# Kernel optimization log

Hardware: AMD Instinct MI355X
Metric: run time of the kernel (lower is better)

Reference implementation:

```python
import jax, jax.numpy as jnp
import numpy as np

ALPHA = 0.2  # LeakyReLU negative slope
NEG_INF = -9e15


def _gat_layer(Wh, adj, a, concat):
    """One GraphAttentionLayer given pre-projected Wh [B,N,F].
    Algebraic split of the concat attention: e[b,i,j] = lrelu(Wh[i]@a1 + Wh[j]@a2),
    identical math to matmul(cat(Wh_i, Wh_j), a)."""
    F_ = Wh.shape[-1]
    f1 = Wh @ a[:F_, 0]   # [B,N]
    f2 = Wh @ a[F_:, 0]   # [B,N]
    e = jax.nn.leaky_relu(f1[:, :, None] + f2[:, None, :], negative_slope=ALPHA)  # [B,N,N]
    e = jnp.where(adj > 0, e, NEG_INF)
    att = jax.nn.softmax(e, axis=-1)            # dropout omitted (eval mode)
    h_prime = jnp.einsum('bij,bjf->bif', att, Wh)
    return jax.nn.elu(h_prime) if concat else h_prime


def setup_inputs() -> dict:
    key = jax.random.key(0)
    ks = jax.random.split(key, 9)
    B, N, Fin, H, nH, Fout = 4, 2048, 512, 128, 4, 256
    x = jax.random.normal(ks[0], (B, N, Fin), dtype=jnp.float32)
    adj = jax.random.randint(ks[1], (B, N, N), 0, 2, dtype=jnp.int32)
    mask = jnp.ones((B, N), dtype=jnp.float32)
    s = 0.05
    W_heads = jax.random.normal(ks[2], (nH, Fin, H), dtype=jnp.float32) * s
    a_heads = jax.random.normal(ks[3], (nH, 2 * H, 1), dtype=jnp.float32) * s
    W_out = jax.random.normal(ks[4], (nH * H, Fout), dtype=jnp.float32) * s
    a_out = jax.random.normal(ks[5], (2 * Fout, 1), dtype=jnp.float32) * s
    W_pool = jax.random.normal(ks[6], (Fout, Fout), dtype=jnp.float32) * s
    b_pool = jax.random.normal(ks[7], (Fout,), dtype=jnp.float32) * s
    return {"x": x, "adj": adj, "mask": mask, "W_heads": W_heads, "a_heads": a_heads,
            "W_out": W_out, "a_out": a_out, "W_pool": W_pool, "b_pool": b_pool}


def reference(x, adj, mask, W_heads, a_heads, W_out, a_out, W_pool, b_pool):
    # multi-head GAT layer, heads concatenated (dropout = identity in eval)
    heads = [_gat_layer(x @ W_heads[h], adj, a_heads[h], concat=True)
             for h in range(W_heads.shape[0])]
    xcat = jnp.concatenate(heads, axis=-1)                 # [B,N,nH*H]
    x_out = _gat_layer(xcat @ W_out, adj, a_out, concat=False)  # [B,N,Fout]
    x_out = x_out * mask[:, :, None]
    pooled = x_out.sum(axis=1) / (mask.sum(axis=1, keepdims=True) + 1e-10)
    graph_embedding = jax.nn.relu(pooled @ W_pool + b_pool)
    return graph_embedding, x_out
```

## Files before the change

kernel.cpp:

```cpp
#include <hip/hip_runtime.h>

typedef unsigned short u16;
typedef __attribute__((ext_vector_type(8))) short s8v;
typedef __attribute__((ext_vector_type(8))) unsigned short us8;
typedef __attribute__((ext_vector_type(4))) float f4v;

#define L2E 1.4426950408889634f

typedef __attribute__((address_space(1))) void gvoid_t;
typedef __attribute__((address_space(3))) void lvoid_t;

__device__ __forceinline__ u16 f2bf(float f) {
  unsigned u = __builtin_bit_cast(unsigned, f);
  return (u16)((u + 0x7FFFu + ((u >> 16) & 1u)) >> 16);
}
__device__ __forceinline__ float bf2f(u16 h) {
  return __builtin_bit_cast(float, ((unsigned)h) << 16);
}
__device__ __forceinline__ f4v mfma16(s8v a, s8v b, f4v c) {
  return __builtin_amdgcn_mfma_f32_16x16x32_bf16(a, b, c, 0, 0, 0);
}
__device__ __forceinline__ float exp2fast(float x) {
#if __has_builtin(__builtin_amdgcn_exp2f)
  return __builtin_amdgcn_exp2f(x);
#else
  return exp2f(x);
#endif
}
__device__ __forceinline__ void stage16(const u16* g, u16* lds_arr, int slot) {
#if __has_builtin(__builtin_amdgcn_global_load_lds)
  __builtin_amdgcn_global_load_lds((gvoid_t*)(g),
      (lvoid_t*)(lds_arr + (size_t)(slot & ~63) * 8), 16, 0, 0);
#else
  *(us8*)(lds_arr + (size_t)slot * 8) = *(const us8*)g;
#endif
}

__global__ __launch_bounds__(256) void prep_x(const float* __restrict__ x,
                                              u16* __restrict__ xb) {
  int i = (blockIdx.x * 256 + threadIdx.x) * 8;
  float4 v0 = *(const float4*)(x + i);
  float4 v1 = *(const float4*)(x + i + 4);
  us8 o;
  o[0] = f2bf(v0.x); o[1] = f2bf(v0.y); o[2] = f2bf(v0.z); o[3] = f2bf(v0.w);
  o[4] = f2bf(v1.x); o[5] = f2bf(v1.y); o[6] = f2bf(v1.z); o[7] = f2bf(v1.w);
  *(us8*)(xb + i) = o;
}

__global__ __launch_bounds__(256) void prep_wall(const float* __restrict__ W,
                                                 u16* __restrict__ Wt) {
  int idx = blockIdx.x * 256 + threadIdx.x;
  int h = idx >> 16, k = (idx >> 7) & 511, f = idx & 127;
  Wt[(size_t)(h * 128 + f) * 512 + k] = f2bf(W[idx]);
}
__global__ __launch_bounds__(256) void prep_wout(const float* __restrict__ W,
                                                 u16* __restrict__ Wt) {
  int idx = blockIdx.x * 256 + threadIdx.x;
  int k = idx >> 8, c = idx & 255;
  Wt[(size_t)c * 512 + k] = f2bf(W[idx]);
}
__global__ __launch_bounds__(256) void prep_adj(const int* __restrict__ adj,
                                                unsigned* __restrict__ adjw) {
  int chunk = blockIdx.x * 4 + (threadIdx.x >> 6);
  int l = threadIdx.x & 63;
  int v = adj[(size_t)chunk * 64 + l];
  unsigned long long m = __ballot(v != 0);
  if (l == 0) {
    ((uint2*)adjw)[chunk] = make_uint2((unsigned)m, (unsigned)(m >> 32));
  }
}

__global__ __launch_bounds__(256) void gemm_bf16(const u16* __restrict__ A,
                                                 const u16* __restrict__ Bt,
                                                 u16* __restrict__ Ct, int CO) {
  const int K = 512, N = 2048;
  int m0 = blockIdx.x * 128;
  int n0 = blockIdx.y * 128;
  int t = threadIdx.x;
  int w = t >> 6, l = t & 63, lr = l & 15, lq = l >> 4;
  int wr = w >> 1, wc = w & 1;
  __shared__ u16 As[2][128 * 32];
  __shared__ u16 Bs[2][128 * 32];
  f4v zero4 = {0.f, 0.f, 0.f, 0.f};
  f4v acc[4][4];
#pragma unroll
  for (int i = 0; i < 4; ++i)
#pragma unroll
    for (int j = 0; j < 4; ++j) acc[i][j] = zero4;

  auto stage = [&](int buf, int kt) {
    int k0 = kt * 32;
    int row = t >> 2, ch = t & 3;
    stage16(A + (size_t)(m0 + row) * K + k0 + ch * 8, As[buf], t);
    stage16(Bt + (size_t)(n0 + row) * K + k0 + ch * 8, Bs[buf], t);
    int s2 = t + 256;
    row = s2 >> 2; ch = s2 & 3;
    stage16(A + (size_t)(m0 + row) * K + k0 + ch * 8, As[buf], s2);
    stage16(Bt + (size_t)(n0 + row) * K + k0 + ch * 8, Bs[buf], s2);
  };
  stage(0, 0);
  for (int kt = 0; kt < 16; ++kt) {
    __syncthreads();
    if (kt < 15) stage((kt + 1) & 1, kt + 1);
    const u16* as = As[kt & 1];
    const u16* bs = Bs[kt & 1];
    s8v af[4], bfr[4];
#pragma unroll
    for (int rf = 0; rf < 4; ++rf)
      af[rf] = *(const s8v*)&as[(wr * 64 + rf * 16 + lr) * 32 + lq * 8];
#pragma unroll
    for (int nf = 0; nf < 4; ++nf)
      bfr[nf] = *(const s8v*)&bs[(wc * 64 + nf * 16 + lr) * 32 + lq * 8];
#pragma unroll
    for (int rf = 0; rf < 4; ++rf)
#pragma unroll
      for (int nf = 0; nf < 4; ++nf)
        acc[rf][nf] = mfma16(af[rf], bfr[nf], acc[rf][nf]);
  }
  int bidx = m0 >> 11;
  int nr0 = m0 & 2047;
#pragma unroll
  for (int rf = 0; rf < 4; ++rf) {
#pragma unroll
    for (int nf = 0; nf < 4; ++nf) {
      int col = n0 + wc * 64 + nf * 16 + lr;
      int nr = nr0 + wr * 64 + rf * 16 + lq * 4;
      f4v a = acc[rf][nf];
      ushort4 v = make_ushort4(f2bf(a[0]), f2bf(a[1]), f2bf(a[2]), f2bf(a[3]));
      *(ushort4*)&Ct[((size_t)bidx * CO + col) * N + nr] = v;
    }
  }
}

__global__ __launch_bounds__(256) void fkern(const u16* __restrict__ Wht,
                                             const float* __restrict__ a,
                                             float* __restrict__ f1L,
                                             float* __restrict__ f2L, int COLS,
                                             int F) {
  const int N = 2048;
  int h = blockIdx.z, b = blockIdx.y;
  int nl = threadIdx.x & 63, fc = threadIdx.x >> 6;
  int n = blockIdx.x * 64 + nl;
  int F4 = F >> 2;
  const u16* colp = Wht + ((size_t)(b * COLS + h * F + fc * F4)) * N + n;
  const float* ah = a + h * 2 * F + fc * F4;
  float a1 = 0.f, a2 = 0.f;
  for (int c = 0; c < F4; ++c) {
    float v = bf2f(colp[(size_t)c * N]);
    a1 = fmaf(v, ah[c], a1);
    a2 = fmaf(v, ah[F + c], a2);
  }
  __shared__ float r1[4][64], r2[4][64];
  r1[fc][nl] = a1;
  r2[fc][nl] = a2;
  __syncthreads();
  if (fc == 0) {
    float s1 = r1[0][nl] + r1[1][nl] + r1[2][nl] + r1[3][nl];
    float s2 = r2[0][nl] + r2[1][nl] + r2[2][nl] + r2[3][nl];
    f1L[(size_t)(h * 4 + b) * N + n] = s1 * L2E;
    f2L[(size_t)(h * 4 + b) * N + n] = s2 * L2E;
  }
}

__global__ __launch_bounds__(256) void fmax_kern(const float* __restrict__ f2L,
                                                 float* __restrict__ f2m) {
  int row = blockIdx.x;
  const float* p = f2L + (size_t)row * 2048;
  int t = threadIdx.x;
  float v = -__builtin_inff();
  for (int k = 0; k < 8; ++k) v = fmaxf(v, p[t + k * 256]);
#pragma unroll
  for (int d = 1; d < 64; d <<= 1) v = fmaxf(v, __shfl_xor(v, d));
  __shared__ float wm[4];
  if ((t & 63) == 0) wm[t >> 6] = v;
  __syncthreads();
  if (t == 0) f2m[row] = fmaxf(fmaxf(wm[0], wm[1]), fmaxf(wm[2], wm[3]));
}

template <int CT, bool ELU>
__global__ __launch_bounds__(256, 2) void attn_kernel(
    const u16* __restrict__ Wht, const float* __restrict__ f1L,
    const float* __restrict__ f2L, const float* __restrict__ f2max,
    const unsigned* __restrict__ adjw, const float* __restrict__ mask,
    void* __restrict__ outp) {
  const int N = 2048;
  constexpr int NCH = CT / 128;
  constexpr int ROWS = 64;
  constexpr int NT = 2048 / ROWS;
  constexpr int FHD = (CT == 512) ? 1 : 0;
  int kb = blockIdx.x;
  int x = kb & 7, g = kb >> 3;
  int p = x + 8 * (g / NT);
  int it = g % NT;
  int b = p / NCH, ch = p % NCH;
  int i0 = it * ROWS, col0 = ch * 128;
  int fh = FHD ? ch : 0;
  int t = threadIdx.x;
  int w = t >> 6, l = t & 63, lr = l & 15, lq = l >> 4;

  __shared__ u16 Vs[2][128 * 64];
  __shared__ unsigned adjs[ROWS * 65];
  __shared__ float f2s[2048];

  const float* f1p = f1L + (size_t)(fh * 4 + b) * N + i0;
  const float* f2p = f2L + (size_t)(fh * 4 + b) * N;
  float f2m = f2max[fh * 4 + b];
  float f1v = f1p[w * 16 + lr];
  float su = f1v + f2m;
  float M = fmaxf(su, 0.2f * su);
  float c1 = f1v - M;
  float c2 = 0.2f * f1v - M;
  const u16* vbase = Wht + (size_t)(b * CT + col0) * 2048;

  for (int i = t; i < ROWS * 64; i += 256) {
    int row = i >> 6, wd = i & 63;
    adjs[row * 65 + wd] = adjw[(size_t)(b * N + i0 + row) * 64 + wd];
  }
  for (int i = t; i < 2048; i += 256) f2s[i] = f2p[i];

  auto stage = [&](int buf, int kt) {
    int k0 = kt * 64;
#pragma unroll
    for (int j2 = 0; j2 < 4; ++j2) {
      int s = j2 * 256 + t;
      int c = s >> 3, q = s & 7;
      stage16(vbase + (size_t)c * 2048 + k0 + q * 8, Vs[buf], s);
    }
  };
  stage(0, 0);

  f4v zero4 = {0.f, 0.f, 0.f, 0.f};
  f4v acc[8];
#pragma unroll
  for (int j = 0; j < 8; ++j) acc[j] = zero4;
  float s_ = 0.f;

  for (int kt = 0; kt < 32; ++kt) {
    __syncthreads();
    if (kt < 31) stage((kt + 1) & 1, kt + 1);
    const u16* vs = Vs[kt & 1];
#pragma unroll
    for (int kk = 0; kk < 2; ++kk) {
      int jt = kt * 2 + kk;
      s8v vf[8];
#pragma unroll
      for (int nf = 0; nf < 8; ++nf)
        vf[nf] = *(const s8v*)&vs[(nf * 16 + lr) * 64 + kk * 32 + lq * 8];
      float4 fa = *(const float4*)&f2s[jt * 32 + lq * 8];
      float4 fb = *(const float4*)&f2s[jt * 32 + lq * 8 + 4];
      float f2c[8] = {fa.x, fa.y, fa.z, fa.w, fb.x, fb.y, fb.z, fb.w};
      unsigned aw = adjs[(w * 16 + lr) * 65 + jt];
      union { s8v v; unsigned u[4]; } pk;
#pragma unroll
      for (int ep = 0; ep < 4; ++ep) {
        float t1 = c1 + f2c[2 * ep];
        float t2 = fmaf(0.2f, f2c[2 * ep], c2);
        float p0 = exp2fast(fmaxf(t1, t2));
        p0 = ((aw >> (lq * 8 + 2 * ep)) & 1u) ? p0 : 0.f;
        s_ += p0;
        float t3 = c1 + f2c[2 * ep + 1];
        float t4 = fmaf(0.2f, f2c[2 * ep + 1], c2);
        float p1 = exp2fast(fmaxf(t3, t4));
        p1 = ((aw >> (lq * 8 + 2 * ep + 1)) & 1u) ? p1 : 0.f;
        s_ += p1;
        asm("v_cvt_pk_bf16_f32 %0, %1, %2"
            : "=v"(pk.u[ep]) : "v"(p0), "v"(p1));
      }
      s8v pa = pk.v;
#pragma unroll
      for (int nf = 0; nf < 8; ++nf)
        acc[nf] = mfma16(pa, vf[nf], acc[nf]);
    }
  }
  s_ += __shfl_xor(s_, 16);
  s_ += __shfl_xor(s_, 32);
  float inv = 1.f / fmaxf(s_, 1e-30f);
  f4v i4;
#pragma unroll
  for (int r = 0; r < 4; ++r) i4[r] = __shfl(inv, lq * 4 + r);
  int rowb = i0 + w * 16 + lq * 4;
#pragma unroll
  for (int nf = 0; nf < 8; ++nf) {
    int col = col0 + nf * 16 + lr;
#pragma unroll
    for (int r = 0; r < 4; ++r) {
      float v = acc[nf][r] * i4[r];
      size_t ob = (size_t)(b * N + rowb + r) * CT + col;
      if constexpr (ELU) {
        v = v > 0.f ? v : exp2fast(v * L2E) - 1.f;
        ((u16*)outp)[ob] = f2bf(v);
      } else {
        ((float*)outp)[ob] = v * mask[b * N + rowb + r];
      }
    }
  }
}

__global__ __launch_bounds__(256) void pool1(const float* __restrict__ xout,
                                             const float* __restrict__ mask,
                                             float* __restrict__ pool,
                                             float* __restrict__ den) {
  int b = blockIdx.x >> 6, s = blockIdx.x & 63;
  int c = threadIdx.x;
  int n0 = s * 32;
  float acc = 0.f;
  for (int r = 0; r < 32; ++r)
    acc += xout[((size_t)(b * 2048 + n0 + r)) * 256 + c];
  atomicAdd(&pool[b * 256 + c], acc);
  if (c == 0) {
    float ms = 0.f;
    for (int r = 0; r < 32; ++r) ms += mask[b * 2048 + n0 + r];
    atomicAdd(&den[b], ms);
  }
}
__global__ __launch_bounds__(256) void pool2(const float* __restrict__ pool,
                                             const float* __restrict__ den,
                                             const float* __restrict__ Wp,
                                             const float* __restrict__ bp,
                                             float* __restrict__ out) {
  int b = blockIdx.x, f = threadIdx.x;
  __shared__ float pv[256];
  float inv = 1.f / (den[b] + 1e-10f);
  pv[f] = pool[b * 256 + f] * inv;
  __syncthreads();
  float acc = bp[f];
  for (int c = 0; c < 256; ++c) acc = fmaf(pv[c], Wp[c * 256 + f], acc);
  out[b * 256 + f] = fmaxf(acc, 0.f);
}

extern "C" void kernel_launch(void* const* d_in, const int* in_sizes, int n_in,
                              void* d_out, int out_size, void* d_ws,
                              size_t ws_size, hipStream_t stream) {
  (void)in_sizes; (void)n_in; (void)out_size; (void)ws_size;
  const float* x = (const float*)d_in[0];
  const int* adj = (const int*)d_in[1];
  const float* mask = (const float*)d_in[2];
  const float* Whds = (const float*)d_in[3];
  const float* ahds = (const float*)d_in[4];
  const float* Wout = (const float*)d_in[5];
  const float* aout = (const float*)d_in[6];
  const float* Wpool = (const float*)d_in[7];
  const float* bpool = (const float*)d_in[8];
  float* out = (float*)d_out;

  char* ws = (char*)d_ws;
  size_t off = 0;
  auto take = [&](size_t n) {
    char* p = ws + off;
    off += (n + 255) & ~(size_t)255;
    return p;
  };
  u16* xb = (u16*)take(8192ull * 512 * 2);
  u16* Wta = (u16*)take(512ull * 512 * 2);
  u16* Wto = (u16*)take(256ull * 512 * 2);
  unsigned* adjw = (unsigned*)take(4ull * 2048 * 64 * 4);
  u16* Wht = (u16*)take(4ull * 512 * 2048 * 2);
  float* f1a = (float*)take(4ull * 4 * 2048 * 4);
  float* f2a = (float*)take(4ull * 4 * 2048 * 4);
  u16* xcat = (u16*)take(8192ull * 512 * 2);
  u16* Wh2t = (u16*)take(4ull * 256 * 2048 * 2);
  float* f1b = (float*)take(4ull * 2048 * 4);
  float* f2b = (float*)take(4ull * 2048 * 4);
  float* f2ma = (float*)take(16 * 4);
  float* f2mb = (float*)take(4 * 4);
  float* pool = (float*)take(1024 * 4);
  float* den = (float*)take(256);

  prep_x<<<2048, 256, 0, stream>>>(x, xb);
  prep_wall<<<1024, 256, 0, stream>>>(Whds, Wta);
  prep_wout<<<512, 256, 0, stream>>>(Wout, Wto);
  prep_adj<<<65536, 256, 0, stream>>>(adj, adjw);
  gemm_bf16<<<dim3(64, 4), 256, 0, stream>>>(xb, Wta, Wht, 512);
  fkern<<<dim3(32, 4, 4), 256, 0, stream>>>(Wht, ahds, f1a, f2a, 512, 128);
  fmax_kern<<<16, 256, 0, stream>>>(f2a, f2ma);
  attn_kernel<512, true><<<512, 256, 0, stream>>>(Wht, f1a, f2a, f2ma,
                                                  adjw, nullptr, xcat);
  gemm_bf16<<<dim3(64, 2), 256, 0, stream>>>(xcat, Wto, Wh2t, 256);
  fkern<<<dim3(32, 4, 1), 256, 0, stream>>>(Wh2t, aout, f1b, f2b, 256, 256);
  fmax_kern<<<4, 256, 0, stream>>>(f2b, f2mb);
  attn_kernel<256, false><<<256, 256, 0, stream>>>(Wh2t, f1b, f2b, f2mb,
                                                   adjw, mask, out + 1024);
  hipMemsetAsync(pool, 0, 4096 + 256, stream);
  pool1<<<256, 256, 0, stream>>>(out + 1024, mask, pool, den);
  pool2<<<4, 256, 0, stream>>>(pool, den, Wpool, bpool, out);
}
```

Baseline: 196.4 us.

## Split attention over the neighbour dimension across wave groups and swizzle LDS tiles

The attention kernel now runs 512-thread blocks in which groups of waves each handle a slice of the neighbour (j) range for the same rows. Partial accumulators and row sums are combined through LDS atomics before normalisation and a vectorised store. The second-layer attention now launches 512 blocks with fewer rows each, to raise parallelism. Both the GEMM and the attention V tiles use an XOR swizzle on the 16-byte chunk index to avoid LDS bank conflicts, and f2 is read straight from global memory instead of being staged in LDS. The costs are the extra reduction step, the LDS atomics and more LDS per block.

```diff
diff --git a/kernel.cpp b/kernel.cpp
--- a/kernel.cpp
+++ b/kernel.cpp
@@ -91,14 +91,17 @@
   auto stage = [&](int buf, int kt) {
     int k0 = kt * 32;
     int row = t >> 2, ch = t & 3;
-    stage16(A + (size_t)(m0 + row) * K + k0 + ch * 8, As[buf], t);
-    stage16(Bt + (size_t)(n0 + row) * K + k0 + ch * 8, Bs[buf], t);
+    int q = (ch ^ ((row >> 1) & 3)) * 8;
+    stage16(A + (size_t)(m0 + row) * K + k0 + q, As[buf], t);
+    stage16(Bt + (size_t)(n0 + row) * K + k0 + q, Bs[buf], t);
     int s2 = t + 256;
     row = s2 >> 2; ch = s2 & 3;
-    stage16(A + (size_t)(m0 + row) * K + k0 + ch * 8, As[buf], s2);
-    stage16(Bt + (size_t)(n0 + row) * K + k0 + ch * 8, Bs[buf], s2);
+    q = (ch ^ ((row >> 1) & 3)) * 8;
+    stage16(A + (size_t)(m0 + row) * K + k0 + q, As[buf], s2);
+    stage16(Bt + (size_t)(n0 + row) * K + k0 + q, Bs[buf], s2);
   };
   stage(0, 0);
+  int swz = (lq ^ ((lr >> 1) & 3)) * 8;
   for (int kt = 0; kt < 16; ++kt) {
     __syncthreads();
     if (kt < 15) stage((kt + 1) & 1, kt + 1);
@@ -107,10 +110,10 @@
     s8v af[4], bfr[4];
 #pragma unroll
     for (int rf = 0; rf < 4; ++rf)
-      af[rf] = *(const s8v*)&as[(wr * 64 + rf * 16 + lr) * 32 + lq * 8];
+      af[rf] = *(const s8v*)&as[(wr * 64 + rf * 16 + lr) * 32 + swz];
 #pragma unroll
     for (int nf = 0; nf < 4; ++nf)
-      bfr[nf] = *(const s8v*)&bs[(wc * 64 + nf * 16 + lr) * 32 + lq * 8];
+      bfr[nf] = *(const s8v*)&bs[(wc * 64 + nf * 16 + lr) * 32 + swz];
 #pragma unroll
     for (int rf = 0; rf < 4; ++rf)
 #pragma unroll
@@ -177,16 +180,19 @@
   if (t == 0) f2m[row] = fmaxf(fmaxf(wm[0], wm[1]), fmaxf(wm[2], wm[3]));
 }
 
-template <int CT, bool ELU>
-__global__ __launch_bounds__(256, 2) void attn_kernel(
+template <int CT, int WPJ, bool ELU>
+__global__ __launch_bounds__(512, 4) void attn_kernel(
     const u16* __restrict__ Wht, const float* __restrict__ f1L,
     const float* __restrict__ f2L, const float* __restrict__ f2max,
     const unsigned* __restrict__ adjw, const float* __restrict__ mask,
     void* __restrict__ outp) {
   const int N = 2048;
   constexpr int NCH = CT / 128;
-  constexpr int ROWS = 64;
+  constexpr int ROWS = WPJ * 16;
   constexpr int NT = 2048 / ROWS;
+  constexpr int NJ = 8 / WPJ;
+  constexpr int JR = 2048 / NJ;
+  constexpr int KT = JR / 32;
   constexpr int FHD = (CT == 512) ? 1 : 0;
   int kb = blockIdx.x;
   int x = kb & 7, g = kb >> 3;
@@ -197,34 +203,40 @@
   int fh = FHD ? ch : 0;
   int t = threadIdx.x;
   int w = t >> 6, l = t & 63, lr = l & 15, lq = l >> 4;
-
-  __shared__ u16 Vs[2][128 * 64];
+  int jg = w / WPJ, ws = w % WPJ;
+  int tg = t & (WPJ * 64 - 1);
+
+  __shared__ __attribute__((aligned(16))) u16 Vs[NJ * 2 * 4096];
   __shared__ unsigned adjs[ROWS * 65];
-  __shared__ float f2s[2048];
+  __shared__ float sum_lds[ROWS];
+  float* accm = (float*)Vs;
 
   const float* f1p = f1L + (size_t)(fh * 4 + b) * N + i0;
   const float* f2p = f2L + (size_t)(fh * 4 + b) * N;
   float f2m = f2max[fh * 4 + b];
-  float f1v = f1p[w * 16 + lr];
+  float f1v = f1p[ws * 16 + lr];
   float su = f1v + f2m;
   float M = fmaxf(su, 0.2f * su);
   float c1 = f1v - M;
   float c2 = 0.2f * f1v - M;
   const u16* vbase = Wht + (size_t)(b * CT + col0) * 2048;
-
-  for (int i = t; i < ROWS * 64; i += 256) {
+  int j0g = jg * JR;
+
+  for (int i = t; i < ROWS * 64; i += 512) {
     int row = i >> 6, wd = i & 63;
     adjs[row * 65 + wd] = adjw[(size_t)(b * N + i0 + row) * 64 + wd];
   }
-  for (int i = t; i < 2048; i += 256) f2s[i] = f2p[i];
-
+  u16* vg0 = &Vs[(jg * 2 + 0) * 4096];
+  u16* vg1 = &Vs[(jg * 2 + 1) * 4096];
   auto stage = [&](int buf, int kt) {
-    int k0 = kt * 64;
-#pragma unroll
-    for (int j2 = 0; j2 < 4; ++j2) {
-      int s = j2 * 256 + t;
-      int c = s >> 3, q = s & 7;
-      stage16(vbase + (size_t)c * 2048 + k0 + q * 8, Vs[buf], s);
+    u16* dst = buf ? vg1 : vg0;
+    int k0 = j0g + kt * 32;
+#pragma unroll
+    for (int j2 = 0; j2 < 512 / (WPJ * 64); ++j2) {
+      int s = j2 * (WPJ * 64) + tg;
+      int c = s >> 2, q = s & 3;
+      stage16(vbase + (size_t)c * 2048 + k0 + (q ^ ((c >> 1) & 3)) * 8, dst,
+              s);
     }
   };
   stage(0, 0);
@@ -234,64 +246,82 @@
 #pragma unroll
   for (int j = 0; j < 8; ++j) acc[j] = zero4;
   float s_ = 0.f;
-
-  for (int kt = 0; kt < 32; ++kt) {
+  int chn = lq ^ ((lr >> 1) & 3);
+
+  for (int kt = 0; kt < KT; ++kt) {
     __syncthreads();
-    if (kt < 31) stage((kt + 1) & 1, kt + 1);
-    const u16* vs = Vs[kt & 1];
-#pragma unroll
-    for (int kk = 0; kk < 2; ++kk) {
-      int jt = kt * 2 + kk;
-      s8v vf[8];
-#pragma unroll
-      for (int nf = 0; nf < 8; ++nf)
-        vf[nf] = *(const s8v*)&vs[(nf * 16 + lr) * 64 + kk * 32 + lq * 8];
-      float4 fa = *(const float4*)&f2s[jt * 32 + lq * 8];
-      float4 fb = *(const float4*)&f2s[jt * 32 + lq * 8 + 4];
-      float f2c[8] = {fa.x, fa.y, fa.z, fa.w, fb.x, fb.y, fb.z, fb.w};
-      unsigned aw = adjs[(w * 16 + lr) * 65 + jt];
-      union { s8v v; unsigned u[4]; } pk;
-#pragma unroll
-      for (int ep = 0; ep < 4; ++ep) {
-        float t1 = c1 + f2c[2 * ep];
-        float t2 = fmaf(0.2f, f2c[2 * ep], c2);
-        float p0 = exp2fast(fmaxf(t1, t2));
-        p0 = ((aw >> (lq * 8 + 2 * ep)) & 1u) ? p0 : 0.f;
-        s_ += p0;
-        float t3 = c1 + f2c[2 * ep + 1];
-        float t4 = fmaf(0.2f, f2c[2 * ep + 1], c2);
-        float p1 = exp2fast(fmaxf(t3, t4));
-        p1 = ((aw >> (lq * 8 + 2 * ep + 1)) & 1u) ? p1 : 0.f;
-        s_ += p1;
-        asm("v_cvt_pk_bf16_f32 %0, %1, %2"
-            : "=v"(pk.u[ep]) : "v"(p0), "v"(p1));
-      }
-      s8v pa = pk.v;
-#pragma unroll
-      for (int nf = 0; nf < 8; ++nf)
-        acc[nf] = mfma16(pa, vf[nf], acc[nf]);
+    if (kt < KT - 1) stage((kt + 1) & 1, kt + 1);
+    const u16* vs = (kt & 1) ? vg1 : vg0;
+    s8v vf[8];
+#pragma unroll
+    for (int nf = 0; nf < 8; ++nf)
+      vf[nf] = *(const s8v*)&vs[(nf * 16 + lr) * 32 + chn * 8];
+    float4 fa = *(const float4*)&f2p[j0g + kt * 32 + lq * 8];
+    float4 fb = *(const float4*)&f2p[j0g + kt * 32 + lq * 8 + 4];
+    float f2c[8] = {fa.x, fa.y, fa.z, fa.w, fb.x, fb.y, fb.z, fb.w};
+    unsigned aw = adjs[(ws * 16 + lr) * 65 + jg * KT + kt];
+    union { s8v v; unsigned u[4]; } pk;
+#pragma unroll
+    for (int ep = 0; ep < 4; ++ep) {
+      float t1 = c1 + f2c[2 * ep];
+      float t2 = fmaf(0.2f, f2c[2 * ep], c2);
+      float p0 = exp2fast(fmaxf(t1, t2));
+      p0 = ((aw >> (lq * 8 + 2 * ep)) & 1u) ? p0 : 0.f;
+      s_ += p0;
+      float t3 = c1 + f2c[2 * ep + 1];
+      float t4 = fmaf(0.2f, f2c[2 * ep + 1], c2);
+      float p1 = exp2fast(fmaxf(t3, t4));
+      p1 = ((aw >> (lq * 8 + 2 * ep + 1)) & 1u) ? p1 : 0.f;
+      s_ += p1;
+      asm("v_cvt_pk_bf16_f32 %0, %1, %2"
+          : "=v"(pk.u[ep]) : "v"(p0), "v"(p1));
     }
+    s8v pa = pk.v;
+#pragma unroll
+    for (int nf = 0; nf < 8; ++nf)
+      acc[nf] = mfma16(pa, vf[nf], acc[nf]);
   }
   s_ += __shfl_xor(s_, 16);
   s_ += __shfl_xor(s_, 32);
-  float inv = 1.f / fmaxf(s_, 1e-30f);
-  f4v i4;
-#pragma unroll
-  for (int r = 0; r < 4; ++r) i4[r] = __shfl(inv, lq * 4 + r);
-  int rowb = i0 + w * 16 + lq * 4;
-#pragma unroll
-  for (int nf = 0; nf < 8; ++nf) {
-    int col = col0 + nf * 16 + lr;
-#pragma unroll
-    for (int r = 0; r < 4; ++r) {
-      float v = acc[nf][r] * i4[r];
-      size_t ob = (size_t)(b * N + rowb + r) * CT + col;
-      if constexpr (ELU) {
-        v = v > 0.f ? v : exp2fast(v * L2E) - 1.f;
-        ((u16*)outp)[ob] = f2bf(v);
-      } else {
-        ((float*)outp)[ob] = v * mask[b * N + rowb + r];
-      }
+
+  __syncthreads();
+  if (jg == 0) {
+    if (l < 16) sum_lds[ws * 16 + lr] = s_;
+#pragma unroll
+    for (int nf = 0; nf < 8; ++nf)
+#pragma unroll
+      for (int r = 0; r < 4; ++r)
+        accm[(ws * 16 + lq * 4 + r) * 128 + nf * 16 + lr] = acc[nf][r];
+  }
+  __syncthreads();
+  if (jg > 0) {
+    if (l < 16) atomicAdd(&sum_lds[ws * 16 + lr], s_);
+#pragma unroll
+    for (int nf = 0; nf < 8; ++nf)
+#pragma unroll
+      for (int r = 0; r < 4; ++r)
+        atomicAdd(&accm[(ws * 16 + lq * 4 + r) * 128 + nf * 16 + lr],
+                  acc[nf][r]);
+  }
+  __syncthreads();
+#pragma unroll
+  for (int e = 0; e < WPJ * 2; ++e) {
+    int pid = e * 512 + t;
+    int row = pid >> 6, cp = (pid & 63) * 2;
+    float S = sum_lds[row];
+    float inv = 1.f / fmaxf(S, 1e-30f);
+    float2 vv = *(const float2*)&accm[row * 128 + cp];
+    float v0 = vv.x * inv;
+    float v1 = vv.y * inv;
+    size_t ob = (size_t)(b * N + i0 + row) * CT + col0 + cp;
+    if constexpr (ELU) {
+      v0 = v0 > 0.f ? v0 : exp2fast(v0 * L2E) - 1.f;
+      v1 = v1 > 0.f ? v1 : exp2fast(v1 * L2E) - 1.f;
+      unsigned pkk = (unsigned)f2bf(v0) | ((unsigned)f2bf(v1) << 16);
+      *(unsigned*)((u16*)outp + ob) = pkk;
+    } else {
+      float mk = mask[b * N + i0 + row];
+      *(float2*)((float*)outp + ob) = make_float2(v0 * mk, v1 * mk);
     }
   }
 }
@@ -373,13 +403,13 @@
   gemm_bf16<<<dim3(64, 4), 256, 0, stream>>>(xb, Wta, Wht, 512);
   fkern<<<dim3(32, 4, 4), 256, 0, stream>>>(Wht, ahds, f1a, f2a, 512, 128);
   fmax_kern<<<16, 256, 0, stream>>>(f2a, f2ma);
-  attn_kernel<512, true><<<512, 256, 0, stream>>>(Wht, f1a, f2a, f2ma,
-                                                  adjw, nullptr, xcat);
+  attn_kernel<512, 4, true><<<512, 512, 0, stream>>>(Wht, f1a, f2a, f2ma,
+                                                     adjw, nullptr, xcat);
   gemm_bf16<<<dim3(64, 2), 256, 0, stream>>>(xcat, Wto, Wh2t, 256);
   fkern<<<dim3(32, 4, 1), 256, 0, stream>>>(Wh2t, aout, f1b, f2b, 256, 256);
   fmax_kern<<<4, 256, 0, stream>>>(f2b, f2mb);
-  attn_kernel<256, false><<<256, 256, 0, stream>>>(Wh2t, f1b, f2b, f2mb,
-                                                   adjw, mask, out + 1024);
+  attn_kernel<256, 2, false><<<512, 512, 0, stream>>>(Wh2t, f1b, f2b, f2mb,
+                                                      adjw, mask, out + 1024);
   hipMemsetAsync(pool, 0, 4096 + 256, stream);
   pool1<<<256, 256, 0, stream>>>(out + 1024, mask, pool, den);
   pool2<<<4, 256, 0, stream>>>(pool, den, Wpool, bpool, out);
```

Result: slower. 222.6 us (+13.4%).
